# Optimization experiments

Measured on AMD Instinct MI355X. Metric: run time of the kernel, lower is better.

The kernel has to match this reference:

```python
import jax, jax.numpy as jnp
import numpy as np


def _ring_mask(n, d, dtype):
    # concentric-square mask: ring index r = min(i, j, n-1-i, n-1-j);
    # outer d rings are 0, inner rings are 1; center forced to 1.
    i = jnp.arange(n)
    ri = jnp.minimum(i, n - 1 - i)  # [n]
    ring = jnp.minimum(ri[:, None], ri[None, :])  # [n, n]
    mask = (ring >= d).astype(dtype)
    w = (n + 1) // 2
    mask = mask.at[w - 1, w - 1].set(jnp.asarray(1, dtype))
    return mask


def _conv2d(x, w, b):
    # x: [B,1,2,C], w: [1,1,2,k] -> [B,1,1,C] (padding only along last axis)
    pad = (w.shape[3] - 1) // 2
    y = jax.lax.conv_general_dilated(
        x, w, window_strides=(1, 1), padding=((0, 0), (pad, pad)),
        dimension_numbers=('NCHW', 'OIHW', 'NCHW'))
    return y + b.reshape(1, 1, 1, 1)


def setup_inputs() -> dict:
    key = jax.random.key(0)
    k1, k2, k3, k4, k5 = jax.random.split(key, 5)
    B, C1, C2, P = 512, 16, 30, 15
    K = 5  # int((log2(480)+3)/2) made odd
    x = jax.random.normal(k1, (B, C1, C2, P, P), dtype=jnp.float32)
    w1 = jax.random.normal(k2, (1, 1, 2, K), dtype=jnp.float32) * 0.3
    b1 = jax.random.normal(k3, (1,), dtype=jnp.float32) * 0.1
    w2 = jax.random.normal(k4, (1, 1, 2, K), dtype=jnp.float32) * 0.3
    b2 = jax.random.normal(k5, (1,), dtype=jnp.float32) * 0.1
    return {"x": x, "w1": w1, "b1": b1, "w2": w2, "b2": b2}


def reference(x, w1, b1, w2, b2):
    B, C1, C2, H, W = x.shape
    C = C1 * C2
    out = x.reshape(B, C, H, W)
    d = (W - 1) // 2 - 1  # patch_size == W, ScaleMaskModule d
    mask = _ring_mask(W, d, x.dtype)  # [W, W]

    # masked branch: adaptive avg pool(1) == spatial mean of masked input
    out_x1 = (out * mask).mean(axis=(2, 3))  # [B, C]
    out_x2 = out_x1[:, ::-1]                 # reversed channel order
    out_xx = jnp.stack([out_x1, out_x2], axis=1)[:, None]  # [B,1,2,C]

    # plain branch
    out1 = out.mean(axis=(2, 3))  # [B, C]
    out2 = out1[:, ::-1]
    outx = jnp.stack([out1, out2], axis=1)[:, None]  # [B,1,2,C]

    a1 = jax.nn.sigmoid(_conv2d(outx, w1, b1))    # [B,1,1,C]
    a2 = jax.nn.sigmoid(_conv2d(out_xx, w2, b2))  # [B,1,1,C]
    at1 = jnp.transpose(a1 * a2, (0, 3, 1, 2))    # [B,C,1,1]
    at = jax.nn.sigmoid((at1 - 0.2) * 2)

    out = out * at
    return out.reshape(B, C1, C2, H, W)
```

## Files before the change

### kernel.cpp

```cpp
#include <hip/hip_runtime.h>
#include <math.h>

#define BB 512
#define CC 480
#define HW 225
#define NCH (BB*CC)

__global__ __launch_bounds__(256) void means_kernel(
    const float* __restrict__ x, float* __restrict__ M, float* __restrict__ R)
{
    const int wave = threadIdx.x >> 6;
    const int lane = threadIdx.x & 63;
    const long long ch = (long long)blockIdx.x * 4 + wave;
    if (ch >= NCH) return;
    const float* base = x + ch * HW;

    float full = 0.f, ring = 0.f;
#pragma unroll
    for (int j = 0; j < 4; ++j) {
        int idx = lane + 64 * j;
        if (idx < HW) {
            float v = base[idx];
            full += v;
            int h = idx / 15, w = idx - h * 15;
            if (h >= 6 && h <= 8 && w >= 6 && w <= 8) ring += v;
        }
    }
#pragma unroll
    for (int off = 32; off > 0; off >>= 1) {
        full += __shfl_down(full, off, 64);
        ring += __shfl_down(ring, off, 64);
    }
    if (lane == 0) {
        M[ch] = full * (1.0f / 225.0f);
        R[ch] = ring * (1.0f / 225.0f);
    }
}

__device__ __forceinline__ float sigmoidf(float v) {
    return 1.0f / (1.0f + __expf(-v));
}

__global__ __launch_bounds__(256) void scale_kernel(
    const float* __restrict__ x,
    const float* __restrict__ M, const float* __restrict__ R,
    const float* __restrict__ w1, const float* __restrict__ b1,
    const float* __restrict__ w2, const float* __restrict__ b2,
    float* __restrict__ out)
{
    const int wave = threadIdx.x >> 6;
    const int lane = threadIdx.x & 63;
    const long long ch = (long long)blockIdx.x * 4 + wave;
    if (ch >= NCH) return;
    const int b = (int)(ch / CC);
    const int c = (int)(ch - (long long)b * CC);

    const float* Mb = M + (long long)b * CC;
    const float* Rb = R + (long long)b * CC;

    float g1 = b1[0], g2 = b2[0];
#pragma unroll
    for (int k = 0; k < 5; ++k) {
        int j = c + k - 2;
        if (j >= 0 && j < CC) {
            g1 += w1[k] * Mb[j] + w1[5 + k] * Mb[CC - 1 - j];
            g2 += w2[k] * Rb[j] + w2[5 + k] * Rb[CC - 1 - j];
        }
    }
    const float a1 = sigmoidf(g1);
    const float a2 = sigmoidf(g2);
    const float at = sigmoidf((a1 * a2 - 0.2f) * 2.0f);

    const float* bx = x + ch * HW;
    float* bo = out + ch * HW;
#pragma unroll
    for (int j = 0; j < 4; ++j) {
        int idx = lane + 64 * j;
        if (idx < HW) bo[idx] = bx[idx] * at;
    }
}

extern "C" void kernel_launch(void* const* d_in, const int* in_sizes, int n_in,
                              void* d_out, int out_size, void* d_ws, size_t ws_size,
                              hipStream_t stream)
{
    const float* x  = (const float*)d_in[0];
    const float* w1 = (const float*)d_in[1];
    const float* b1 = (const float*)d_in[2];
    const float* w2 = (const float*)d_in[3];
    const float* b2 = (const float*)d_in[4];
    float* out = (float*)d_out;

    float* M = (float*)d_ws;
    float* R = M + NCH;

    const int blocks = NCH / 4;
    means_kernel<<<blocks, 256, 0, stream>>>(x, M, R);
    scale_kernel<<<blocks, 256, 0, stream>>>(x, M, R, w1, b1, w2, b2, out);
}
```

Measured before the change: 484.7 us.

## Fuse means and scale into one per-batch kernel with float4 loads

Replaces the two kernels with a single kernel that uses one 1024-thread block per batch item. The block computes the channel means and ring means into shared memory, then computes the attention scales, then rescales the batch slice. Loads are vectorised to float4 and output is written with nontemporal stores. The intent is to drop the second launch and the global M/R round trip, and to have the second read of x hit L2 (about 432 KB per batch). The cost is only 512 blocks with per-element index arithmetic in the reduction, which may limit occupancy and bandwidth.

```diff
diff --git a/kernel.cpp b/kernel.cpp
--- a/kernel.cpp
+++ b/kernel.cpp
@@ -4,79 +4,117 @@
 #define BB 512
 #define CC 480
 #define HW 225
-#define NCH (BB*CC)
+#define CHW (CC * HW)
+#define NF4 (CHW / 4)
+#define NGRP (CC / 4)
+#define NTHREADS 1024
+#define NWAVES (NTHREADS / 64)
 
-__global__ __launch_bounds__(256) void means_kernel(
-    const float* __restrict__ x, float* __restrict__ M, float* __restrict__ R)
-{
-    const int wave = threadIdx.x >> 6;
-    const int lane = threadIdx.x & 63;
-    const long long ch = (long long)blockIdx.x * 4 + wave;
-    if (ch >= NCH) return;
-    const float* base = x + ch * HW;
-
-    float full = 0.f, ring = 0.f;
-#pragma unroll
-    for (int j = 0; j < 4; ++j) {
-        int idx = lane + 64 * j;
-        if (idx < HW) {
-            float v = base[idx];
-            full += v;
-            int h = idx / 15, w = idx - h * 15;
-            if (h >= 6 && h <= 8 && w >= 6 && w <= 8) ring += v;
-        }
-    }
-#pragma unroll
-    for (int off = 32; off > 0; off >>= 1) {
-        full += __shfl_down(full, off, 64);
-        ring += __shfl_down(ring, off, 64);
-    }
-    if (lane == 0) {
-        M[ch] = full * (1.0f / 225.0f);
-        R[ch] = ring * (1.0f / 225.0f);
-    }
-}
+using f4 = __attribute__((ext_vector_type(4))) float;
 
 __device__ __forceinline__ float sigmoidf(float v) {
     return 1.0f / (1.0f + __expf(-v));
 }
 
-__global__ __launch_bounds__(256) void scale_kernel(
+__global__ __launch_bounds__(NTHREADS) void fused_kernel(
     const float* __restrict__ x,
-    const float* __restrict__ M, const float* __restrict__ R,
     const float* __restrict__ w1, const float* __restrict__ b1,
     const float* __restrict__ w2, const float* __restrict__ b2,
     float* __restrict__ out)
 {
-    const int wave = threadIdx.x >> 6;
-    const int lane = threadIdx.x & 63;
-    const long long ch = (long long)blockIdx.x * 4 + wave;
-    if (ch >= NCH) return;
-    const int b = (int)(ch / CC);
-    const int c = (int)(ch - (long long)b * CC);
+    __shared__ float Ms[CC];
+    __shared__ float Rs[CC];
+    __shared__ float As[CC];
 
-    const float* Mb = M + (long long)b * CC;
-    const float* Rb = R + (long long)b * CC;
+    const int b = blockIdx.x;
+    const int t = threadIdx.x;
+    const int wave = t >> 6;
+    const int lane = t & 63;
 
-    float g1 = b1[0], g2 = b2[0];
+    const f4* __restrict__ xb4 = (const f4*)(x + (long long)b * CHW);
+
+    for (int gr = wave; gr < NGRP; gr += NWAVES) {
+        const f4* gp = xb4 + gr * 225;
+        float f0 = 0.f, f1 = 0.f, f2 = 0.f, f3 = 0.f;
+        float r0 = 0.f, r1 = 0.f, r2 = 0.f, r3 = 0.f;
 #pragma unroll
-    for (int k = 0; k < 5; ++k) {
-        int j = c + k - 2;
-        if (j >= 0 && j < CC) {
-            g1 += w1[k] * Mb[j] + w1[5 + k] * Mb[CC - 1 - j];
-            g2 += w2[k] * Rb[j] + w2[5 + k] * Rb[CC - 1 - j];
+        for (int j = 0; j < 4; ++j) {
+            const int idx = lane + 64 * j;
+            if (idx < 225) {
+                f4 v = gp[idx];
+                const int e0 = 4 * idx;
+#pragma unroll
+                for (int jj = 0; jj < 4; ++jj) {
+                    const int e = e0 + jj;
+                    const float vv = v[jj];
+                    const int q = (e >= 450) ? ((e >= 675) ? 3 : 2)
+                                             : ((e >= 225) ? 1 : 0);
+                    const int r = e - 225 * q;
+                    const bool ring = (r >= 96 && r <= 98) ||
+                                      (r >= 111 && r <= 113) ||
+                                      (r >= 126 && r <= 128);
+                    const float rv = ring ? vv : 0.f;
+                    f0 += (q == 0) ? vv : 0.f;
+                    f1 += (q == 1) ? vv : 0.f;
+                    f2 += (q == 2) ? vv : 0.f;
+                    f3 += (q == 3) ? vv : 0.f;
+                    r0 += (q == 0) ? rv : 0.f;
+                    r1 += (q == 1) ? rv : 0.f;
+                    r2 += (q == 2) ? rv : 0.f;
+                    r3 += (q == 3) ? rv : 0.f;
+                }
+            }
+        }
+#pragma unroll
+        for (int off = 32; off > 0; off >>= 1) {
+            f0 += __shfl_down(f0, off, 64);
+            f1 += __shfl_down(f1, off, 64);
+            f2 += __shfl_down(f2, off, 64);
+            f3 += __shfl_down(f3, off, 64);
+            r0 += __shfl_down(r0, off, 64);
+            r1 += __shfl_down(r1, off, 64);
+            r2 += __shfl_down(r2, off, 64);
+            r3 += __shfl_down(r3, off, 64);
+        }
+        if (lane == 0) {
+            const float s = 1.0f / 225.0f;
+            Ms[4 * gr + 0] = f0 * s;  Rs[4 * gr + 0] = r0 * s;
+            Ms[4 * gr + 1] = f1 * s;  Rs[4 * gr + 1] = r1 * s;
+            Ms[4 * gr + 2] = f2 * s;  Rs[4 * gr + 2] = r2 * s;
+            Ms[4 * gr + 3] = f3 * s;  Rs[4 * gr + 3] = r3 * s;
         }
     }
-    const float a1 = sigmoidf(g1);
-    const float a2 = sigmoidf(g2);
-    const float at = sigmoidf((a1 * a2 - 0.2f) * 2.0f);
+    __syncthreads();
 
-    const float* bx = x + ch * HW;
-    float* bo = out + ch * HW;
+    if (t < CC) {
+        const int c = t;
+        float g1 = b1[0], g2 = b2[0];
 #pragma unroll
-    for (int j = 0; j < 4; ++j) {
-        int idx = lane + 64 * j;
-        if (idx < HW) bo[idx] = bx[idx] * at;
+        for (int k = 0; k < 5; ++k) {
+            const int j = c + k - 2;
+            if (j >= 0 && j < CC) {
+                g1 += w1[k] * Ms[j] + w1[5 + k] * Ms[CC - 1 - j];
+                g2 += w2[k] * Rs[j] + w2[5 + k] * Rs[CC - 1 - j];
+            }
+        }
+        As[c] = sigmoidf((sigmoidf(g1) * sigmoidf(g2) - 0.2f) * 2.0f);
+    }
+    __syncthreads();
+
+    f4* __restrict__ ob4 = (f4*)(out + (long long)b * CHW);
+    for (int g = t; g < NF4; g += NTHREADS) {
+        f4 v = xb4[g];
+        const int e0 = 4 * g;
+        const int c0 = e0 / 225;
+        const int rr = e0 - 225 * c0;
+        const int c1 = c0 + (rr >= 224);
+        const int c2 = c0 + (rr >= 223);
+        const int c3 = c0 + (rr >= 222);
+        v[0] *= As[c0];
+        v[1] *= As[c1];
+        v[2] *= As[c2];
+        v[3] *= As[c3];
+        __builtin_nontemporal_store(v, &ob4[g]);
     }
 }
 
@@ -91,10 +129,5 @@
     const float* b2 = (const float*)d_in[4];
     float* out = (float*)d_out;
 
-    float* M = (float*)d_ws;
-    float* R = M + NCH;
-
-    const int blocks = NCH / 4;
-    means_kernel<<<blocks, 256, 0, stream>>>(x, M, R);
-    scale_kernel<<<blocks, 256, 0, stream>>>(x, M, R, w1, b1, w2, b2, out);
+    fused_kernel<<<BB, NTHREADS, 0, stream>>>(x, w1, b1, w2, b2, out);
 }
```

After: 403.4 us. 16.8% less time.
